# Performance work log

Measured on AMD Instinct MI355X. Metric: run time of the kernel, lower is better.

The kernel has to match this reference:

```python
import jax, jax.numpy as jnp
import numpy as np

N_NODES = 100000
N_EDGES = 3200000
N_FEAT = 512
NHID = 256
LATENT = 64

def _spmm(edge_index, edge_weight, h, num_nodes):
    # out[dst] = sum_e w_e * h[src_e]  (sparse adj @ h)
    src, dst = edge_index[0], edge_index[1]
    msgs = edge_weight[:, None] * h[src]            # [E, D]
    return jax.ops.segment_sum(msgs, dst, num_segments=num_nodes)

def _gcn_conv(x, edge_index, edge_weight, W, b, num_nodes):
    # GCNConv: adj @ (x @ W) + b
    return _spmm(edge_index, edge_weight, x @ W, num_nodes) + b

def setup_inputs() -> dict:
    key = jax.random.key(0)
    ks = jax.random.split(key, 8)
    x = jax.random.normal(ks[0], (N_NODES, N_FEAT), dtype=jnp.float32)
    edge_index = jax.random.randint(ks[1], (2, N_EDGES), 0, N_NODES, dtype=jnp.int32)
    edge_weight = jax.random.uniform(ks[2], (N_EDGES,), dtype=jnp.float32)
    s1 = 1.0 / np.sqrt(N_FEAT)
    s2 = 1.0 / np.sqrt(NHID)
    W1 = jax.random.normal(ks[3], (N_FEAT, NHID), dtype=jnp.float32) * s1
    b1 = jnp.zeros((NHID,), dtype=jnp.float32)
    W_mu = jax.random.normal(ks[4], (NHID, LATENT), dtype=jnp.float32) * s2
    b_mu = jnp.zeros((LATENT,), dtype=jnp.float32)
    W_logvar = jax.random.normal(ks[5], (NHID, LATENT), dtype=jnp.float32) * s2
    b_logvar = jnp.zeros((LATENT,), dtype=jnp.float32)
    return {"x": x, "edge_index": edge_index, "edge_weight": edge_weight,
            "W1": W1, "b1": b1, "W_mu": W_mu, "b_mu": b_mu,
            "W_logvar": W_logvar, "b_logvar": b_logvar}

def reference(x, edge_index, edge_weight, W1, b1, W_mu, b_mu, W_logvar, b_logvar):
    n = x.shape[0]
    # dropout is identity in eval mode (training=False)
    h = jax.nn.relu(_gcn_conv(x, edge_index, edge_weight, W1, b1, n))  # [N, nhid]
    mu = _gcn_conv(h, edge_index, edge_weight, W_mu, b_mu, n)          # [N, latent]
    logvar = _gcn_conv(h, edge_index, edge_weight, W_logvar, b_logvar, n)
    return (mu, logvar)
```

## Files before the change

### kernel.cpp

```cpp
#include <hip/hip_runtime.h>
#include <hip/hip_bf16.h>

#define NN 100000
#define NE 3200000
#define NF 512
#define NH 256
#define NL 64
#define PAD 40

#define NBKT 250
#define NPB 400
#define CAP 13600

typedef __bf16 bf16x8 __attribute__((ext_vector_type(8)));
typedef __bf16 bf16x4 __attribute__((ext_vector_type(4)));
typedef __bf16 bf16x2 __attribute__((ext_vector_type(2)));
typedef float  f32x4  __attribute__((ext_vector_type(4)));

__global__ void k_binit2(int* __restrict__ bcur) {
    int t = threadIdx.x;
    if (t < NBKT) bcur[t * 16] = t * CAP;
}

__global__ __launch_bounds__(256) void k_bucket0(const int* __restrict__ src,
                                                 const int* __restrict__ dst,
                                                 const int* __restrict__ wbits,
                                                 int* __restrict__ bcur,
                                                 int2* __restrict__ stage_sw,
                                                 int* __restrict__ stage_d) {
    __shared__ int cnt[NBKT];
    __shared__ int base[NBKT];
    int tid = threadIdx.x;
    if (tid < NBKT) cnt[tid] = 0;
    __syncthreads();
    int e0 = blockIdx.x * 1024;
    int ss[4], ww[4], dd[4], lr[4], bb[4];
#pragma unroll
    for (int k = 0; k < 4; k++) {
        int e = e0 + k * 256 + tid;
        int d = dst[e];
        ss[k] = src[e];
        ww[k] = wbits[e];
        dd[k] = d;
        bb[k] = (int)((unsigned)d / NPB);
        lr[k] = atomicAdd(&cnt[bb[k]], 1);
    }
    __syncthreads();
    if (tid < NBKT) base[tid] = atomicAdd(&bcur[tid * 16], cnt[tid]);
    __syncthreads();
#pragma unroll
    for (int k = 0; k < 4; k++) {
        int pos = base[bb[k]] + lr[k];
        stage_sw[pos] = make_int2(ss[k], ww[k]);
        stage_d[pos] = dd[k];
    }
}

__global__ void k_bscan(const int* __restrict__ bcur, int* __restrict__ bstart) {
    __shared__ int s[256];
    int t = threadIdx.x;
    int v = (t < NBKT) ? (bcur[t * 16] - t * CAP) : 0;
    s[t] = v;
    __syncthreads();
    for (int off = 1; off < 256; off <<= 1) {
        int a = (t >= off) ? s[t - off] : 0;
        __syncthreads();
        s[t] += a;
        __syncthreads();
    }
    if (t < NBKT) bstart[t] = s[t] - v;
}

__global__ __launch_bounds__(512) void k_build(const int2* __restrict__ stage_sw,
                                               const int* __restrict__ stage_d,
                                               const int* __restrict__ bcur,
                                               const int* __restrict__ bstart,
                                               int* __restrict__ deg,
                                               int* __restrict__ row_ptr,
                                               int2* __restrict__ sedge) {
    __shared__ int hist[NPB];
    __shared__ int sb[2][512];
    int b = blockIdx.x;
    int t = threadIdx.x;
    int n0 = b * NPB;
    int s0 = b * CAP;
    int fill = bcur[b * 16] - s0;

    if (t < NPB) hist[t] = 0;
    __syncthreads();
    for (int i = t; i < fill; i += 512)
        atomicAdd(&hist[stage_d[s0 + i] - n0], 1);
    __syncthreads();
    int v = (t < NPB) ? hist[t] : 0;
    int buf = 0;
    sb[0][t] = v;
    __syncthreads();
    for (int off = 1; off < 512; off <<= 1) {
        int nv = sb[buf][t] + ((t >= off) ? sb[buf][t - off] : 0);
        buf ^= 1;
        sb[buf][t] = nv;
        __syncthreads();
    }
    int base = bstart[b];
    if (t < NPB) {
        int abs0 = base + sb[buf][t] - v;
        deg[n0 + t] = v;
        row_ptr[n0 + t] = abs0;
        hist[t] = abs0;
    }
    __syncthreads();
    for (int i = t; i < fill; i += 512) {
        int dl = stage_d[s0 + i] - n0;
        int pos = atomicAdd(&hist[dl], 1);
        sedge[pos] = stage_sw[s0 + i];
    }
}

__global__ void k_packW1(const float* __restrict__ W, __bf16* __restrict__ P) {
    int i = blockIdx.x * 256 + threadIdx.x;
    int j = i & 7, l = (i >> 3) & 63, kc = (i >> 9) & 15, nt = i >> 13;
    int k = kc * 32 + (l >> 4) * 8 + j;
    int n = nt * 16 + (l & 15);
    P[i] = (__bf16)W[k * NH + n];
}

__global__ void k_packW2(const float* __restrict__ Wmu, const float* __restrict__ Wlv,
                         __bf16* __restrict__ P) {
    int i = blockIdx.x * 256 + threadIdx.x;
    int j = i & 7, l = (i >> 3) & 63, kc = (i >> 9) & 7, nt = i >> 12;
    int k = kc * 32 + (l >> 4) * 8 + j;
    int n = nt * 16 + (l & 15);
    float v = (n < NL) ? Wmu[k * NL + n] : Wlv[k * NL + (n - NL)];
    P[i] = (__bf16)v;
}

__global__ __launch_bounds__(256) void k_gemm1(const float* __restrict__ x,
                                               const __bf16* __restrict__ Wp,
                                               __bf16* __restrict__ T) {
    __shared__ __bf16 As[64 * PAD];
    int tid = threadIdx.x;
    int wv = tid >> 6, lane = tid & 63;
    int quad = lane >> 4, l16 = lane & 15;
    long m0 = (long)blockIdx.x * 64;

    int srow = tid >> 2;
    int scol = (tid & 3) * 8;
    long grow = m0 + srow; if (grow > NN - 1) grow = NN - 1;
    const float* xrow = x + grow * NF;

    f32x4 acc[4][4];
#pragma unroll
    for (int a = 0; a < 4; a++)
#pragma unroll
        for (int b = 0; b < 4; b++) acc[a][b] = (f32x4)0.f;

    float4 p0 = *(const float4*)(xrow + scol);
    float4 p1 = *(const float4*)(xrow + scol + 4);

    for (int kc = 0; kc < 16; kc++) {
        union { bf16x8 v; __bf16 e[8]; } u;
        u.e[0] = (__bf16)p0.x; u.e[1] = (__bf16)p0.y;
        u.e[2] = (__bf16)p0.z; u.e[3] = (__bf16)p0.w;
        u.e[4] = (__bf16)p1.x; u.e[5] = (__bf16)p1.y;
        u.e[6] = (__bf16)p1.z; u.e[7] = (__bf16)p1.w;
        *(bf16x8*)&As[srow * PAD + scol] = u.v;
        __syncthreads();
        if (kc < 15) {
            p0 = *(const float4*)(xrow + (kc + 1) * 32 + scol);
            p1 = *(const float4*)(xrow + (kc + 1) * 32 + scol + 4);
        }
        bf16x8 bfr[4];
#pragma unroll
        for (int nt = 0; nt < 4; nt++)
            bfr[nt] = *(const bf16x8*)(Wp + (((long)(wv * 4 + nt) * 16 + kc) * 64 + lane) * 8);
#pragma unroll
        for (int mt = 0; mt < 4; mt++) {
            bf16x8 af = *(const bf16x8*)&As[(mt * 16 + l16) * PAD + quad * 8];
#pragma unroll
            for (int nt = 0; nt < 4; nt++)
                acc[mt][nt] = __builtin_amdgcn_mfma_f32_16x16x32_bf16(af, bfr[nt], acc[mt][nt], 0, 0, 0);
        }
        __syncthreads();
    }
#pragma unroll
    for (int mt = 0; mt < 4; mt++)
#pragma unroll
        for (int r = 0; r < 4; r++) {
            long gr = m0 + mt * 16 + quad * 4 + r;
            if (gr < NN) {
#pragma unroll
                for (int nt = 0; nt < 4; nt++)
                    T[gr * 256 + wv * 64 + nt * 16 + l16] = (__bf16)acc[mt][nt][r];
            }
        }
}

__global__ __launch_bounds__(256) void k_spmm_h(const __bf16* __restrict__ T,
                                                const int2* __restrict__ sedge,
                                                const int* __restrict__ row_ptr,
                                                const int* __restrict__ deg,
                                                const float* __restrict__ bias,
                                                __bf16* __restrict__ o) {
    int wave = threadIdx.x >> 6, lane = threadIdx.x & 63;
    int n = blockIdx.x * 4 + wave;
    if (n >= NN) return;
    int i = row_ptr[n];
    int end = i + deg[n];
    float a0 = 0.f, a1 = 0.f, a2 = 0.f, a3 = 0.f;
    const bf16x4* base = (const bf16x4*)T;
    for (; i + 16 <= end; i += 16) {
        int2 e[16];
#pragma unroll
        for (int k = 0; k < 16; k++) e[k] = sedge[i + k];
        bf16x4 v[16];
#pragma unroll
        for (int k = 0; k < 16; k++) v[k] = base[(long)e[k].x * 64 + lane];
#pragma unroll
        for (int k = 0; k < 16; k++) {
            float w = __uint_as_float(e[k].y);
            a0 += w * (float)v[k][0];
            a1 += w * (float)v[k][1];
            a2 += w * (float)v[k][2];
            a3 += w * (float)v[k][3];
        }
    }
    for (; i + 4 <= end; i += 4) {
        int2 e[4];
#pragma unroll
        for (int k = 0; k < 4; k++) e[k] = sedge[i + k];
        bf16x4 v[4];
#pragma unroll
        for (int k = 0; k < 4; k++) v[k] = base[(long)e[k].x * 64 + lane];
#pragma unroll
        for (int k = 0; k < 4; k++) {
            float w = __uint_as_float(e[k].y);
            a0 += w * (float)v[k][0];
            a1 += w * (float)v[k][1];
            a2 += w * (float)v[k][2];
            a3 += w * (float)v[k][3];
        }
    }
    for (; i < end; i++) {
        int2 e = sedge[i];
        float w = __uint_as_float(e.y);
        bf16x4 v = base[(long)e.x * 64 + lane];
        a0 += w * (float)v[0]; a1 += w * (float)v[1];
        a2 += w * (float)v[2]; a3 += w * (float)v[3];
    }
    float4 bv = ((const float4*)bias)[lane];
    bf16x4 ov;
    ov[0] = (__bf16)fmaxf(a0 + bv.x, 0.f);
    ov[1] = (__bf16)fmaxf(a1 + bv.y, 0.f);
    ov[2] = (__bf16)fmaxf(a2 + bv.z, 0.f);
    ov[3] = (__bf16)fmaxf(a3 + bv.w, 0.f);
    ((bf16x4*)o)[(long)n * 64 + lane] = ov;
}

__global__ __launch_bounds__(256) void k_gemm2(const __bf16* __restrict__ h,
                                               const __bf16* __restrict__ Wp,
                                               __bf16* __restrict__ HMb) {
    __shared__ __bf16 As[128 * PAD];
    int tid = threadIdx.x;
    int wv = tid >> 6, lane = tid & 63;
    int quad = lane >> 4, l16 = lane & 15;
    int wr = (wv >> 1) * 64, wc = (wv & 1) * 64;
    long m0 = (long)blockIdx.x * 128;

    int srow = tid >> 1;
    int scol = (tid & 1) * 16;
    long grow = m0 + srow; if (grow > NN - 1) grow = NN - 1;

    f32x4 acc[4][4];
#pragma unroll
    for (int a = 0; a < 4; a++)
#pragma unroll
        for (int b = 0; b < 4; b++) acc[a][b] = (f32x4)0.f;

    const __bf16* rH = h + grow * 256;
    bf16x8 p0 = *(const bf16x8*)(rH + scol);
    bf16x8 p1 = *(const bf16x8*)(rH + scol + 8);

    for (int kc = 0; kc < 8; kc++) {
        *(bf16x8*)&As[srow * PAD + scol] = p0;
        *(bf16x8*)&As[srow * PAD + scol + 8] = p1;
        __syncthreads();
        if (kc < 7) {
            const __bf16* nxt = rH + (kc + 1) * 32;
            p0 = *(const bf16x8*)(nxt + scol);
            p1 = *(const bf16x8*)(nxt + scol + 8);
        }
        bf16x8 bfr[4];
#pragma unroll
        for (int nt = 0; nt < 4; nt++) {
            int ntg = (wc >> 4) + nt;
            bfr[nt] = *(const bf16x8*)(Wp + (((long)ntg * 8 + kc) * 64 + lane) * 8);
        }
#pragma unroll
        for (int mt = 0; mt < 4; mt++) {
            bf16x8 af = *(const bf16x8*)&As[(wr + mt * 16 + l16) * PAD + quad * 8];
#pragma unroll
            for (int nt = 0; nt < 4; nt++)
                acc[mt][nt] = __builtin_amdgcn_mfma_f32_16x16x32_bf16(af, bfr[nt], acc[mt][nt], 0, 0, 0);
        }
        __syncthreads();
    }
#pragma unroll
    for (int mt = 0; mt < 4; mt++)
#pragma unroll
        for (int r = 0; r < 4; r++) {
            long gr = m0 + wr + mt * 16 + quad * 4 + r;
            if (gr < NN) {
#pragma unroll
                for (int nt = 0; nt < 4; nt++)
                    HMb[gr * 128 + wc + nt * 16 + l16] = (__bf16)acc[mt][nt][r];
            }
        }
}

__global__ __launch_bounds__(256) void k_spmm2(const __bf16* __restrict__ HMb,
                                               const int2* __restrict__ sedge,
                                               const int* __restrict__ row_ptr,
                                               const int* __restrict__ deg,
                                               const float* __restrict__ bmu,
                                               const float* __restrict__ blv,
                                               float* __restrict__ out) {
    int wave = threadIdx.x >> 6, lane = threadIdx.x & 63;
    int n = blockIdx.x * 4 + wave;
    if (n >= NN) return;
    int i = row_ptr[n];
    int end = i + deg[n];
    float a0 = 0.f, a1 = 0.f;
    const bf16x2* base = (const bf16x2*)HMb;
    for (; i + 16 <= end; i += 16) {
        int2 e[16];
#pragma unroll
        for (int k = 0; k < 16; k++) e[k] = sedge[i + k];
        bf16x2 v[16];
#pragma unroll
        for (int k = 0; k < 16; k++) v[k] = base[(long)e[k].x * 64 + lane];
#pragma unroll
        for (int k = 0; k < 16; k++) {
            float w = __uint_as_float(e[k].y);
            a0 += w * (float)v[k][0];
            a1 += w * (float)v[k][1];
        }
    }
    for (; i + 4 <= end; i += 4) {
        int2 e[4];
#pragma unroll
        for (int k = 0; k < 4; k++) e[k] = sedge[i + k];
        bf16x2 v[4];
#pragma unroll
        for (int k = 0; k < 4; k++) v[k] = base[(long)e[k].x * 64 + lane];
#pragma unroll
        for (int k = 0; k < 4; k++) {
            float w = __uint_as_float(e[k].y);
            a0 += w * (float)v[k][0];
            a1 += w * (float)v[k][1];
        }
    }
    for (; i < end; i++) {
        int2 e = sedge[i];
        float w = __uint_as_float(e.y);
        bf16x2 v = base[(long)e.x * 64 + lane];
        a0 += w * (float)v[0]; a1 += w * (float)v[1];
    }
    if (lane < 32) {
        float2 b = ((const float2*)bmu)[lane];
        float2 o = {a0 + b.x, a1 + b.y};
        ((float2*)out)[(long)n * 32 + lane] = o;
    } else {
        float2 b = ((const float2*)blv)[lane - 32];
        float2 o = {a0 + b.x, a1 + b.y};
        ((float2*)(out + (long)NN * NL))[(long)n * 32 + (lane - 32)] = o;
    }
}

extern "C" void kernel_launch(void* const* d_in, const int* in_sizes, int n_in,
                              void* d_out, int out_size, void* d_ws, size_t ws_size,
                              hipStream_t stream) {
    const float* x   = (const float*)d_in[0];
    const int*   ei  = (const int*)d_in[1];
    const float* ew  = (const float*)d_in[2];
    const float* W1  = (const float*)d_in[3];
    const float* b1  = (const float*)d_in[4];
    const float* Wmu = (const float*)d_in[5];
    const float* bmu = (const float*)d_in[6];
    const float* Wlv = (const float*)d_in[7];
    const float* blv = (const float*)d_in[8];
    float* out = (float*)d_out;

    char* ws = (char*)d_ws;
    __bf16* XW     = (__bf16*)(ws);
    __bf16* h      = (__bf16*)(ws + 51200000);
    __bf16* HMb    = (__bf16*)(ws + 102400000);
    int2*  sedge   = (int2*) (ws + 128000000);
    int*   deg     = (int*)  (ws + 153600000);
    int*   row_ptr = (int*)  (ws + 154000000);
    int*   bcur    = (int*)  (ws + 154400000);
    int*   bstart  = (int*)  (ws + 154800000);
    __bf16* Wp1    = (__bf16*)(ws + 154900000);
    __bf16* Wp2    = (__bf16*)(ws + 155200000);

    int2* stage_sw = (int2*)(ws + 51200000);
    int*  stage_d  = (int*) (ws + 78400000);

    const int* esrc = ei;
    const int* edst = ei + NE;

    k_packW1<<<dim3(512), dim3(256), 0, stream>>>(W1, Wp1);
    k_packW2<<<dim3(128), dim3(256), 0, stream>>>(Wmu, Wlv, Wp2);

    k_binit2<<<dim3(1), dim3(256), 0, stream>>>(bcur);
    k_bucket0<<<dim3(NE / 1024), dim3(256), 0, stream>>>(esrc, edst, (const int*)ew,
                                                         bcur, stage_sw, stage_d);
    k_bscan<<<dim3(1), dim3(256), 0, stream>>>(bcur, bstart);
    k_build<<<dim3(NBKT), dim3(512), 0, stream>>>(stage_sw, stage_d, bcur, bstart,
                                                  deg, row_ptr, sedge);

    k_gemm1<<<dim3((NN + 63) / 64), dim3(256), 0, stream>>>(x, Wp1, XW);
    k_spmm_h<<<dim3((NN + 3) / 4), dim3(256), 0, stream>>>(XW, sedge, row_ptr, deg, b1, h);

    k_gemm2<<<dim3((NN + 127) / 128), dim3(256), 0, stream>>>(h, Wp2, HMb);
    k_spmm2<<<dim3((NN + 3) / 4), dim3(256), 0, stream>>>(HMb, sedge, row_ptr, deg, bmu, blv, out);
}
```

Baseline: 821.4 us.

## Pack dst into staged src bits, enlarge bucket blocks, merge prep kernels

Stores the local destination offset in the upper bits of the staged src index, so the separate stage_d array and its reads and writes go away. The bucketing kernel now handles 12800 edges per block over 250 blocks, counting in a first pass and scattering in a second. This means far fewer global atomics on the bucket cursors, at the cost of reading dst twice and running fewer blocks. The W1 and W2 packing and the bucket-cursor init are merged into one launch to cut launch overhead.

```diff
diff --git a/kernel.cpp b/kernel.cpp
--- a/kernel.cpp
+++ b/kernel.cpp
@@ -11,48 +11,60 @@
 #define NBKT 250
 #define NPB 400
 #define CAP 13600
+#define EPB 12800
 
 typedef __bf16 bf16x8 __attribute__((ext_vector_type(8)));
 typedef __bf16 bf16x4 __attribute__((ext_vector_type(4)));
 typedef __bf16 bf16x2 __attribute__((ext_vector_type(2)));
 typedef float  f32x4  __attribute__((ext_vector_type(4)));
 
-__global__ void k_binit2(int* __restrict__ bcur) {
-    int t = threadIdx.x;
-    if (t < NBKT) bcur[t * 16] = t * CAP;
+__global__ void k_prep(const float* __restrict__ W1, const float* __restrict__ Wmu,
+                       const float* __restrict__ Wlv, __bf16* __restrict__ P1,
+                       __bf16* __restrict__ P2, int* __restrict__ bcur) {
+    int bid = blockIdx.x;
+    int tid = threadIdx.x;
+    if (bid < 512) {
+        int i = bid * 256 + tid;
+        int j = i & 7, l = (i >> 3) & 63, kc = (i >> 9) & 15, nt = i >> 13;
+        int k = kc * 32 + (l >> 4) * 8 + j;
+        int n = nt * 16 + (l & 15);
+        P1[i] = (__bf16)W1[k * NH + n];
+    } else if (bid < 640) {
+        int i = (bid - 512) * 256 + tid;
+        int j = i & 7, l = (i >> 3) & 63, kc = (i >> 9) & 7, nt = i >> 12;
+        int k = kc * 32 + (l >> 4) * 8 + j;
+        int n = nt * 16 + (l & 15);
+        float v = (n < NL) ? Wmu[k * NL + n] : Wlv[k * NL + (n - NL)];
+        P2[i] = (__bf16)v;
+    } else {
+        if (tid < NBKT) bcur[tid * 16] = tid * CAP;
+    }
 }
 
 __global__ __launch_bounds__(256) void k_bucket0(const int* __restrict__ src,
                                                  const int* __restrict__ dst,
                                                  const int* __restrict__ wbits,
                                                  int* __restrict__ bcur,
-                                                 int2* __restrict__ stage_sw,
-                                                 int* __restrict__ stage_d) {
+                                                 int2* __restrict__ stage) {
     __shared__ int cnt[NBKT];
-    __shared__ int base[NBKT];
+    __shared__ int cur[NBKT];
     int tid = threadIdx.x;
+    int e0 = blockIdx.x * EPB;
     if (tid < NBKT) cnt[tid] = 0;
     __syncthreads();
-    int e0 = blockIdx.x * 1024;
-    int ss[4], ww[4], dd[4], lr[4], bb[4];
-#pragma unroll
-    for (int k = 0; k < 4; k++) {
+    for (int k = 0; k < EPB / 256; k++) {
+        int d = dst[e0 + k * 256 + tid];
+        atomicAdd(&cnt[(unsigned)d / NPB], 1);
+    }
+    __syncthreads();
+    if (tid < NBKT) cur[tid] = atomicAdd(&bcur[tid * 16], cnt[tid]);
+    __syncthreads();
+    for (int k = 0; k < EPB / 256; k++) {
         int e = e0 + k * 256 + tid;
         int d = dst[e];
-        ss[k] = src[e];
-        ww[k] = wbits[e];
-        dd[k] = d;
-        bb[k] = (int)((unsigned)d / NPB);
-        lr[k] = atomicAdd(&cnt[bb[k]], 1);
-    }
-    __syncthreads();
-    if (tid < NBKT) base[tid] = atomicAdd(&bcur[tid * 16], cnt[tid]);
-    __syncthreads();
-#pragma unroll
-    for (int k = 0; k < 4; k++) {
-        int pos = base[bb[k]] + lr[k];
-        stage_sw[pos] = make_int2(ss[k], ww[k]);
-        stage_d[pos] = dd[k];
+        int b = (int)((unsigned)d / NPB);
+        int pos = atomicAdd(&cur[b], 1);
+        stage[pos] = make_int2(src[e] | ((d - b * NPB) << 17), wbits[e]);
     }
 }
 
@@ -71,8 +83,7 @@
     if (t < NBKT) bstart[t] = s[t] - v;
 }
 
-__global__ __launch_bounds__(512) void k_build(const int2* __restrict__ stage_sw,
-                                               const int* __restrict__ stage_d,
+__global__ __launch_bounds__(512) void k_build(const int2* __restrict__ stage,
                                                const int* __restrict__ bcur,
                                                const int* __restrict__ bstart,
                                                int* __restrict__ deg,
@@ -89,7 +100,7 @@
     if (t < NPB) hist[t] = 0;
     __syncthreads();
     for (int i = t; i < fill; i += 512)
-        atomicAdd(&hist[stage_d[s0 + i] - n0], 1);
+        atomicAdd(&hist[(unsigned)stage[s0 + i].x >> 17], 1);
     __syncthreads();
     int v = (t < NPB) ? hist[t] : 0;
     int buf = 0;
@@ -110,28 +121,11 @@
     }
     __syncthreads();
     for (int i = t; i < fill; i += 512) {
-        int dl = stage_d[s0 + i] - n0;
+        int2 sv = stage[s0 + i];
+        int dl = (unsigned)sv.x >> 17;
         int pos = atomicAdd(&hist[dl], 1);
-        sedge[pos] = stage_sw[s0 + i];
-    }
-}
-
-__global__ void k_packW1(const float* __restrict__ W, __bf16* __restrict__ P) {
-    int i = blockIdx.x * 256 + threadIdx.x;
-    int j = i & 7, l = (i >> 3) & 63, kc = (i >> 9) & 15, nt = i >> 13;
-    int k = kc * 32 + (l >> 4) * 8 + j;
-    int n = nt * 16 + (l & 15);
-    P[i] = (__bf16)W[k * NH + n];
-}
-
-__global__ void k_packW2(const float* __restrict__ Wmu, const float* __restrict__ Wlv,
-                         __bf16* __restrict__ P) {
-    int i = blockIdx.x * 256 + threadIdx.x;
-    int j = i & 7, l = (i >> 3) & 63, kc = (i >> 9) & 7, nt = i >> 12;
-    int k = kc * 32 + (l >> 4) * 8 + j;
-    int n = nt * 16 + (l & 15);
-    float v = (n < NL) ? Wmu[k * NL + n] : Wlv[k * NL + (n - NL)];
-    P[i] = (__bf16)v;
+        sedge[pos] = make_int2(sv.x & 0x1FFFF, sv.y);
+    }
 }
 
 __global__ __launch_bounds__(256) void k_gemm1(const float* __restrict__ x,
@@ -402,20 +396,17 @@
     __bf16* Wp1    = (__bf16*)(ws + 154900000);
     __bf16* Wp2    = (__bf16*)(ws + 155200000);
 
-    int2* stage_sw = (int2*)(ws + 51200000);
-    int*  stage_d  = (int*) (ws + 78400000);
+    int2* stage = (int2*)(ws + 51200000);
 
     const int* esrc = ei;
     const int* edst = ei + NE;
 
-    k_packW1<<<dim3(512), dim3(256), 0, stream>>>(W1, Wp1);
-    k_packW2<<<dim3(128), dim3(256), 0, stream>>>(Wmu, Wlv, Wp2);
-
-    k_binit2<<<dim3(1), dim3(256), 0, stream>>>(bcur);
-    k_bucket0<<<dim3(NE / 1024), dim3(256), 0, stream>>>(esrc, edst, (const int*)ew,
-                                                         bcur, stage_sw, stage_d);
+    k_prep<<<dim3(641), dim3(256), 0, stream>>>(W1, Wmu, Wlv, Wp1, Wp2, bcur);
+
+    k_bucket0<<<dim3(NBKT), dim3(256), 0, stream>>>(esrc, edst, (const int*)ew,
+                                                    bcur, stage);
     k_bscan<<<dim3(1), dim3(256), 0, stream>>>(bcur, bstart);
-    k_build<<<dim3(NBKT), dim3(512), 0, stream>>>(stage_sw, stage_d, bcur, bstart,
+    k_build<<<dim3(NBKT), dim3(512), 0, stream>>>(stage, bcur, bstart,
                                                   deg, row_ptr, sedge);
 
     k_gemm1<<<dim3((NN + 63) / 64), dim3(256), 0, stream>>>(x, Wp1, XW);
```

Result: faster. 793.5 us (-3.4%).
